# Optimization experiments

Hardware: AMD Instinct MI355X
Metric: run time of the kernel (lower is better)

The kernel has to match this reference:

```python
import jax, jax.numpy as jnp
import numpy as np

N, E, B = 50000, 800000, 128
IN, HID, OUT = 15, 256, 128
EPS = 1e-5


def setup_inputs() -> dict:
    key = jax.random.key(0)
    ks = jax.random.split(key, 16)
    x = jax.random.normal(ks[0], (N, IN), jnp.float32)
    edge_index = jax.random.randint(ks[1], (2, E), 0, N, jnp.int32)
    batch = jnp.sort(jax.random.randint(ks[2], (N,), 0, B, jnp.int32))
    w = lambda k, i, o: jax.random.normal(k, (i, o), jnp.float32) * (1.0 / np.sqrt(i))
    return {
        "x": x, "edge_index": edge_index, "batch": batch,
        "Wl1": w(ks[3], IN, HID), "Wr1": w(ks[4], IN, HID), "b1": jnp.zeros((HID,), jnp.float32),
        "g1": jnp.ones((HID,), jnp.float32), "bt1": jnp.zeros((HID,), jnp.float32),
        "Wl2": w(ks[5], HID, HID), "Wr2": w(ks[6], HID, HID), "b2": jnp.zeros((HID,), jnp.float32),
        "g2": jnp.ones((HID,), jnp.float32), "bt2": jnp.zeros((HID,), jnp.float32),
        "Wl3": w(ks[7], HID, HID), "Wr3": w(ks[8], HID, HID), "b3": jnp.zeros((HID,), jnp.float32),
        "g3": jnp.ones((HID,), jnp.float32), "bt3": jnp.zeros((HID,), jnp.float32),
        "Wl4": w(ks[9], HID, OUT), "Wr4": w(ks[10], HID, OUT), "b4": jnp.zeros((OUT,), jnp.float32),
        "g4": jnp.ones((OUT,), jnp.float32), "bt4": jnp.zeros((OUT,), jnp.float32),
    }


def _sage(x, src, dst, Wl, Wr, b):
    # mean-aggregate source-node features at each target, then two GEMMs
    msg = x[src]                                            # (E, d)
    agg = jax.ops.segment_sum(msg, dst, num_segments=N)     # (N, d)
    cnt = jax.ops.segment_sum(jnp.ones((src.shape[0],), x.dtype), dst, num_segments=N)
    mean = agg / jnp.clip(cnt, 1.0)[:, None]
    return mean @ Wl + x @ Wr + b


def _ln(x, g, b):
    mu = jnp.mean(x, axis=-1, keepdims=True)
    var = jnp.mean(jnp.square(x - mu), axis=-1, keepdims=True)
    return (x - mu) * jax.lax.rsqrt(var + EPS) * g + b


def reference(x, edge_index, batch,
              Wl1, Wr1, b1, g1, bt1,
              Wl2, Wr2, b2, g2, bt2,
              Wl3, Wr3, b3, g3, bt3,
              Wl4, Wr4, b4, g4, bt4):
    src, dst = edge_index[0], edge_index[1]
    gelu = lambda h: jax.nn.gelu(h, approximate=False)
    h = gelu(_ln(_sage(x, src, dst, Wl1, Wr1, b1), g1, bt1))
    h = gelu(_ln(_sage(h, src, dst, Wl2, Wr2, b2), g2, bt2))
    h = gelu(_ln(_sage(h, src, dst, Wl3, Wr3, b3), g3, bt3))
    h = gelu(_ln(_sage(h, src, dst, Wl4, Wr4, b4), g4, bt4))
    # global mean pool per patch
    s = jax.ops.segment_sum(h, batch, num_segments=B)        # (B, out)
    c = jax.ops.segment_sum(jnp.ones((N,), h.dtype), batch, num_segments=B)
    return s / jnp.clip(c, 1.0)[:, None]
```

## Files before the change

kernel.cpp:

```cpp
#include <hip/hip_runtime.h>
#include <math.h>

constexpr int Nn   = 50000;
constexpr int Ee   = 800000;
constexpr int Bb   = 128;
constexpr int INF  = 15;
constexpr int HID  = 256;
constexpr int OUTF = 128;

constexpr int NCB   = (Nn + 255) / 256;
constexpr int CHUNK = 4096;
constexpr int NB1   = (Ee + CHUNK - 1) / CHUNK;
constexpr int SCANN = NCB * NB1;

typedef __attribute__((ext_vector_type(8))) __bf16 bf16x8;
typedef __attribute__((ext_vector_type(4))) float  f32x4;

__device__ __forceinline__ float gelu_f(float v) {
    return 0.5f * v * (1.0f + erff(v * 0.7071067811865475f));
}

__device__ __forceinline__ unsigned short f2bf(float f) {
    union { float f; unsigned int u; } v; v.f = f;
    unsigned int r = v.u + 0x7fffu + ((v.u >> 16) & 1u);
    return (unsigned short)(r >> 16);
}

__device__ __forceinline__ float bflo(unsigned int p) { return __uint_as_float(p << 16); }
__device__ __forceinline__ float bfhi(unsigned int p) { return __uint_as_float(p & 0xffff0000u); }


__global__ void k_sortA(const int* __restrict__ dst, int* __restrict__ Gcnt) {
    __shared__ int cnt[NCB];
    int tid = threadIdx.x, blk = blockIdx.x;
    for (int i = tid; i < NCB; i += 256) cnt[i] = 0;
    __syncthreads();
    int base = blk * CHUNK;
    for (int i = 0; i < CHUNK; i += 256) {
        int e = base + i + tid;
        if (e < Ee) atomicAdd(&cnt[dst[e] >> 8], 1);
    }
    __syncthreads();
    for (int i = tid; i < NCB; i += 256) Gcnt[i * NB1 + blk] = cnt[i];
}

__global__ void k_gscan_partial(const int* __restrict__ in, int* __restrict__ partial, int n) {
    __shared__ int s[256];
    int tid = threadIdx.x, i = blockIdx.x * 256 + tid;
    s[tid] = (i < n) ? in[i] : 0;
    __syncthreads();
    for (int off = 128; off; off >>= 1) {
        if (tid < off) s[tid] += s[tid + off];
        __syncthreads();
    }
    if (tid == 0) partial[blockIdx.x] = s[0];
}

__global__ void k_gscan_mid(int* __restrict__ partial, int nb) {
    __shared__ int s[256];
    int tid = threadIdx.x;
    int v = (tid < nb) ? partial[tid] : 0;
    s[tid] = v;
    __syncthreads();
    for (int off = 1; off < 256; off <<= 1) {
        int t = (tid >= off) ? s[tid - off] : 0;
        __syncthreads();
        s[tid] += t;
        __syncthreads();
    }
    if (tid < nb) partial[tid] = s[tid] - v;
}

__global__ void k_gscan_final(const int* __restrict__ in, const int* __restrict__ partial,
                              int* __restrict__ out, int n) {
    __shared__ int s[256];
    int tid = threadIdx.x, i = blockIdx.x * 256 + tid;
    int v = (i < n) ? in[i] : 0;
    s[tid] = v;
    __syncthreads();
    for (int off = 1; off < 256; off <<= 1) {
        int t = (tid >= off) ? s[tid - off] : 0;
        __syncthreads();
        s[tid] += t;
        __syncthreads();
    }
    if (i < n) out[i] = s[tid] - v + partial[blockIdx.x];
}

__global__ void k_sortC(const int* __restrict__ dst, const int* __restrict__ srcv,
                        const int* __restrict__ Goff, unsigned int* __restrict__ pairs) {
    __shared__ int cur[NCB];
    int tid = threadIdx.x, blk = blockIdx.x;
    for (int i = tid; i < NCB; i += 256) cur[i] = Goff[i * NB1 + blk];
    __syncthreads();
    int base = blk * CHUNK;
    for (int i = 0; i < CHUNK; i += 256) {
        int e = base + i + tid;
        if (e < Ee) {
            int d = dst[e];
            int p = atomicAdd(&cur[d >> 8], 1);
            pairs[p] = ((unsigned int)(d & 255) << 16) | (unsigned int)srcv[e];
        }
    }
}

__global__ void k_sortD(const unsigned int* __restrict__ pairs, const int* __restrict__ Goff,
                        int* __restrict__ offs, int* __restrict__ srcs, float* __restrict__ invc) {
    __shared__ int fcnt[256];
    __shared__ int fbase[256];
    __shared__ int s[256];
    int tid = threadIdx.x, cb = blockIdx.x;
    int cbase = Goff[cb * NB1];
    int cend = (cb + 1 < NCB) ? Goff[(cb + 1) * NB1] : Ee;
    fcnt[tid] = 0;
    __syncthreads();
    for (int e = cbase + tid; e < cend; e += 256)
        atomicAdd(&fcnt[pairs[e] >> 16], 1);
    __syncthreads();
    int v = fcnt[tid];
    s[tid] = v;
    __syncthreads();
    for (int off = 1; off < 256; off <<= 1) {
        int t = (tid >= off) ? s[tid - off] : 0;
        __syncthreads();
        s[tid] += t;
        __syncthreads();
    }
    fbase[tid] = cbase + s[tid] - v;
    int node = cb * 256 + tid;
    if (node < Nn) {
        offs[node] = fbase[tid];
        invc[node] = 1.0f / (float)(v > 1 ? v : 1);
    }
    __syncthreads();
    fcnt[tid] = fbase[tid];
    __syncthreads();
    for (int e = cbase + tid; e < cend; e += 256) {
        unsigned int pv = pairs[e];
        int p = atomicAdd(&fcnt[pv >> 16], 1);
        srcs[p] = (int)(pv & 0xFFFFu);
    }
}

__global__ void k_bsearch(const int* __restrict__ batch, int* __restrict__ boff,
                          int* __restrict__ offs) {
    int b = threadIdx.x;
    if (b <= Bb) {
        int lo = 0, hi = Nn;
        while (lo < hi) {
            int mid = (lo + hi) >> 1;
            if (batch[mid] < b) lo = mid + 1; else hi = mid;
        }
        boff[b] = lo;
    }
    if (b == 0) offs[Nn] = Ee;
}


template <int NOUT>
__global__ void k_prepW(const float* __restrict__ Wl, const float* __restrict__ Wr,
                        uint4* __restrict__ outw) {
    constexpr int NT = NOUT / 16;
    int G = blockIdx.x * 256 + threadIdx.x;
    int per = 2 * NT * 64;
    int S = G / per, rem = G % per;
    int lane = rem & 63, sT = rem >> 6;
    int s = sT / NT, T = sT % NT;
    int q = lane >> 4, m = lane & 15;
    int k0 = S * 64 + s * 32 + q * 8;
    int nc = T * 16 + m;
    union { uint4 u; unsigned short h[8]; } pk;
#pragma unroll
    for (int j = 0; j < 8; j++) {
        int kk = k0 + j;
        float wv = (kk < 256) ? Wl[kk * NOUT + nc] : Wr[(kk - 256) * NOUT + nc];
        pk.h[j] = f2bf(wv);
    }
    outw[G] = pk.u;
}

__global__ void k_prepW1(const float* __restrict__ Wl, const float* __restrict__ Wr,
                         uint4* __restrict__ outw) {
    int G = blockIdx.x * 256 + threadIdx.x;
    int T = G >> 6, lane = G & 63;
    int q = lane >> 4, m = lane & 15;
    int nc = T * 16 + m;
    union { uint4 u; unsigned short h[8]; } pk;
#pragma unroll
    for (int j = 0; j < 8; j++) {
        int k = q * 8 + j;
        float wv;
        if (k < 15)       wv = Wl[k * HID + nc];
        else if (k == 15) wv = 0.0f;
        else if (k < 31)  wv = Wr[(k - 16) * HID + nc];
        else              wv = 0.0f;
        pk.h[j] = f2bf(wv);
    }
    outw[G] = pk.u;
}


__global__ void k_prep1(const float* __restrict__ x, const int* __restrict__ offs,
                        const int* __restrict__ srcs, const float* __restrict__ invc,
                        unsigned short* __restrict__ A1) {
    int node = blockIdx.x * 16 + (threadIdx.x >> 4);
    int f = threadIdx.x & 15;
    int s0 = offs[node], s1 = offs[node + 1];
    float acc = 0.0f;
    for (int i = s0; i < s1; i++) {
        int s = srcs[i];
        if (f < 15) acc += x[s * INF + f];
    }
    unsigned short mv = (f < 15) ? f2bf(acc * invc[node]) : (unsigned short)0;
    unsigned short xv = (f < 15) ? f2bf(x[(size_t)node * INF + f]) : (unsigned short)0;
    A1[(size_t)node * 32 + f] = mv;
    A1[(size_t)node * 32 + 16 + f] = xv;
}


__global__ void k_agg256_bf(const uint4* __restrict__ h4, const int* __restrict__ offs,
                            const int* __restrict__ srcs, const float* __restrict__ invc,
                            uint4* __restrict__ mean4) {
    int node = blockIdx.x * 4 + (threadIdx.x >> 6);
    int lane = threadIdx.x & 63;
    int sub = lane >> 5, q = lane & 31;
    int s0 = offs[node], s1 = offs[node + 1];
    int deg = s1 - s0;
    int dcap = deg < 64 ? deg : 64;
    int myidx = (lane < deg) ? srcs[s0 + lane] : 0;
    float a[8] = {};
    int i = 0;
    for (; i + 4 <= dcap; i += 4) {
        int sA = __shfl(myidx, i + sub);
        int sB = __shfl(myidx, i + 2 + sub);
        uint4 vA = h4[(size_t)sA * 32 + q];
        uint4 vB = h4[(size_t)sB * 32 + q];
        a[0] += bflo(vA.x); a[1] += bfhi(vA.x);
        a[2] += bflo(vA.y); a[3] += bfhi(vA.y);
        a[4] += bflo(vA.z); a[5] += bfhi(vA.z);
        a[6] += bflo(vA.w); a[7] += bfhi(vA.w);
        a[0] += bflo(vB.x); a[1] += bfhi(vB.x);
        a[2] += bflo(vB.y); a[3] += bfhi(vB.y);
        a[4] += bflo(vB.z); a[5] += bfhi(vB.z);
        a[6] += bflo(vB.w); a[7] += bfhi(vB.w);
    }
    if (i + 2 <= dcap) {
        int sA = __shfl(myidx, i + sub);
        uint4 vA = h4[(size_t)sA * 32 + q];
        a[0] += bflo(vA.x); a[1] += bfhi(vA.x);
        a[2] += bflo(vA.y); a[3] += bfhi(vA.y);
        a[4] += bflo(vA.z); a[5] += bfhi(vA.z);
        a[6] += bflo(vA.w); a[7] += bfhi(vA.w);
        i += 2;
    }
    if (i < dcap && sub == 0) {
        int sA = __shfl(myidx, i);
        uint4 vA = h4[(size_t)sA * 32 + q];
        a[0] += bflo(vA.x); a[1] += bfhi(vA.x);
        a[2] += bflo(vA.y); a[3] += bfhi(vA.y);
        a[4] += bflo(vA.z); a[5] += bfhi(vA.z);
        a[6] += bflo(vA.w); a[7] += bfhi(vA.w);
    }
    for (int j = 64; j + 1 < deg; j += 2) {
        int s = srcs[s0 + j + sub];
        uint4 v = h4[(size_t)s * 32 + q];
        a[0] += bflo(v.x); a[1] += bfhi(v.x);
        a[2] += bflo(v.y); a[3] += bfhi(v.y);
        a[4] += bflo(v.z); a[5] += bfhi(v.z);
        a[6] += bflo(v.w); a[7] += bfhi(v.w);
    }
    if (deg > 64 && ((deg - 64) & 1) && sub == 0) {
        int s = srcs[s1 - 1];
        uint4 v = h4[(size_t)s * 32 + q];
        a[0] += bflo(v.x); a[1] += bfhi(v.x);
        a[2] += bflo(v.y); a[3] += bfhi(v.y);
        a[4] += bflo(v.z); a[5] += bfhi(v.z);
        a[6] += bflo(v.w); a[7] += bfhi(v.w);
    }
#pragma unroll
    for (int j = 0; j < 8; j++) a[j] += __shfl_xor(a[j], 32);
    if (sub == 0) {
        float ic = invc[node];
        uint4 o;
        o.x = (unsigned int)f2bf(a[0] * ic) | ((unsigned int)f2bf(a[1] * ic) << 16);
        o.y = (unsigned int)f2bf(a[2] * ic) | ((unsigned int)f2bf(a[3] * ic) << 16);
        o.z = (unsigned int)f2bf(a[4] * ic) | ((unsigned int)f2bf(a[5] * ic) << 16);
        o.w = (unsigned int)f2bf(a[6] * ic) | ((unsigned int)f2bf(a[7] * ic) << 16);
        mean4[(size_t)node * 32 + q] = o;
    }
}


template <int NOUT, bool F32OUT>
__global__ __launch_bounds__(256) void k_gemm_mfma(
    const unsigned short* __restrict__ Am,
    const unsigned short* __restrict__ Ah,
    const uint4* __restrict__ Wfrag,
    const float* __restrict__ bias, const float* __restrict__ g,
    const float* __restrict__ bt, void* __restrict__ outp, int n) {
    constexpr int NT = NOUT / 16;
    constexpr int CT = NT / 4;
    __shared__ float lnbuf[2][4][64];
    int tid = threadIdx.x;
    int w = tid >> 6, lane = tid & 63;
    int q = lane >> 4, m = lane & 15;
    int rowbase = blockIdx.x * 64;

    f32x4 acc[4][CT];
#pragma unroll
    for (int i = 0; i < 4; i++)
#pragma unroll
        for (int t = 0; t < CT; t++) acc[i][t] = (f32x4)0.f;

    union U { uint4 u; bf16x8 b; };
    U a[2][4], b[2][CT];

    auto loadA = [&](int p, U* ar) {
        const unsigned short* A = (p < 8) ? Am : Ah;
        int kk = ((p >> 1) & 3) * 64 + (p & 1) * 32 + q * 8;
#pragma unroll
        for (int i = 0; i < 4; i++)
            ar[i].u = *(const uint4*)(A + (size_t)(rowbase + i * 16 + m) * 256 + kk);
    };
    auto loadB = [&](int p, U* br) {
#pragma unroll
        for (int t = 0; t < CT; t++)
            br[t].u = Wfrag[(size_t)(p * NT + w * CT + t) * 64 + lane];
    };

    loadA(0, a[0]);
    loadB(0, b[0]);
#pragma unroll
    for (int p = 0; p < 16; p++) {
        int cur = p & 1, nxt = cur ^ 1;
        if (p < 15) {
            loadA(p + 1, a[nxt]);
            loadB(p + 1, b[nxt]);
        }
#pragma unroll
        for (int i = 0; i < 4; i++)
#pragma unroll
            for (int t = 0; t < CT; t++)
                acc[i][t] = __builtin_amdgcn_mfma_f32_16x16x32_bf16(
                    a[cur][i].b, b[cur][t].b, acc[i][t], 0, 0, 0);
    }

    int col0 = w * CT * 16;
    float bv[CT], gv[CT], btv[CT];
#pragma unroll
    for (int t = 0; t < CT; t++) {
        int c = col0 + t * 16 + m;
        bv[t] = bias[c]; gv[t] = g[c]; btv[t] = bt[c];
    }
#pragma unroll
    for (int i = 0; i < 4; i++) {
#pragma unroll
        for (int r = 0; r < 4; r++) {
            float s1 = 0.f, s2 = 0.f;
#pragma unroll
            for (int t = 0; t < CT; t++) {
                float v = acc[i][t][r] + bv[t];
                acc[i][t][r] = v;
                s1 += v; s2 += v * v;
            }
#pragma unroll
            for (int o = 1; o < 16; o <<= 1) {
                s1 += __shfl_xor(s1, o);
                s2 += __shfl_xor(s2, o);
            }
            if (m == 0) {
                int row = i * 16 + q * 4 + r;
                lnbuf[0][w][row] = s1;
                lnbuf[1][w][row] = s2;
            }
        }
    }
    __syncthreads();
#pragma unroll
    for (int i = 0; i < 4; i++) {
#pragma unroll
        for (int r = 0; r < 4; r++) {
            int rit = i * 16 + q * 4 + r;
            float ts1 = lnbuf[0][0][rit] + lnbuf[0][1][rit] + lnbuf[0][2][rit] + lnbuf[0][3][rit];
            float ts2 = lnbuf[1][0][rit] + lnbuf[1][1][rit] + lnbuf[1][2][rit] + lnbuf[1][3][rit];
            float mu  = ts1 * (1.0f / NOUT);
            float var = ts2 * (1.0f / NOUT) - mu * mu;
            float rs  = 1.0f / sqrtf(var + 1e-5f);
            int row = rowbase + rit;
            if (row < n) {
#pragma unroll
                for (int t = 0; t < CT; t++) {
                    int c = col0 + t * 16 + m;
                    float y = (acc[i][t][r] - mu) * rs * gv[t] + btv[t];
                    float res = gelu_f(y);
                    if (F32OUT) ((float*)outp)[(size_t)row * NOUT + c] = res;
                    else ((unsigned short*)outp)[(size_t)row * NOUT + c] = f2bf(res);
                }
            }
        }
    }
}


__global__ __launch_bounds__(256) void k_gemm_mfma1(
    const unsigned short* __restrict__ A1, const uint4* __restrict__ Wfrag,
    const float* __restrict__ bias, const float* __restrict__ g,
    const float* __restrict__ bt, unsigned short* __restrict__ outp, int n) {
    constexpr int NT = 16, CT = 4;
    __shared__ float lnbuf[2][4][64];
    int tid = threadIdx.x;
    int w = tid >> 6, lane = tid & 63;
    int q = lane >> 4, m = lane & 15;
    int rowbase = blockIdx.x * 64;

    union U { uint4 u; bf16x8 b; };
    U a[4], b[CT];
#pragma unroll
    for (int i = 0; i < 4; i++) {
        int row = rowbase + i * 16 + m;
        a[i].u = (row < n) ? *(const uint4*)(A1 + (size_t)row * 32 + q * 8)
                           : make_uint4(0u, 0u, 0u, 0u);
    }
#pragma unroll
    for (int t = 0; t < CT; t++)
        b[t].u = Wfrag[(size_t)(w * CT + t) * 64 + lane];

    f32x4 acc[4][CT];
#pragma unroll
    for (int i = 0; i < 4; i++)
#pragma unroll
        for (int t = 0; t < CT; t++)
            acc[i][t] = __builtin_amdgcn_mfma_f32_16x16x32_bf16(
                a[i].b, b[t].b, (f32x4)0.f, 0, 0, 0);

    int col0 = w * CT * 16;
    float bv[CT], gv[CT], btv[CT];
#pragma unroll
    for (int t = 0; t < CT; t++) {
        int c = col0 + t * 16 + m;
        bv[t] = bias[c]; gv[t] = g[c]; btv[t] = bt[c];
    }
#pragma unroll
    for (int i = 0; i < 4; i++) {
#pragma unroll
        for (int r = 0; r < 4; r++) {
            float s1 = 0.f, s2 = 0.f;
#pragma unroll
            for (int t = 0; t < CT; t++) {
                float v = acc[i][t][r] + bv[t];
                acc[i][t][r] = v;
                s1 += v; s2 += v * v;
            }
#pragma unroll
            for (int o = 1; o < 16; o <<= 1) {
                s1 += __shfl_xor(s1, o);
                s2 += __shfl_xor(s2, o);
            }
            if (m == 0) {
                int row = i * 16 + q * 4 + r;
                lnbuf[0][w][row] = s1;
                lnbuf[1][w][row] = s2;
            }
        }
    }
    __syncthreads();
#pragma unroll
    for (int i = 0; i < 4; i++) {
#pragma unroll
        for (int r = 0; r < 4; r++) {
            int rit = i * 16 + q * 4 + r;
            float ts1 = lnbuf[0][0][rit] + lnbuf[0][1][rit] + lnbuf[0][2][rit] + lnbuf[0][3][rit];
            float ts2 = lnbuf[1][0][rit] + lnbuf[1][1][rit] + lnbuf[1][2][rit] + lnbuf[1][3][rit];
            float mu  = ts1 * (1.0f / HID);
            float var = ts2 * (1.0f / HID) - mu * mu;
            float rs  = 1.0f / sqrtf(var + 1e-5f);
            int row = rowbase + rit;
            if (row < n) {
#pragma unroll
                for (int t = 0; t < CT; t++) {
                    int c = col0 + t * 16 + m;
                    float y = (acc[i][t][r] - mu) * rs * gv[t] + btv[t];
                    outp[(size_t)row * HID + c] = f2bf(gelu_f(y));
                }
            }
        }
    }
}


__global__ __launch_bounds__(1024) void k_pool(const float* __restrict__ h,
                                               const int* __restrict__ boff,
                                               float* __restrict__ out) {
    __shared__ float red[8][128];
    int b = blockIdx.x, tid = threadIdx.x;
    int j = tid & 127, grp = tid >> 7;
    int s0 = boff[b], s1 = boff[b + 1];
    float a0 = 0.f, a1 = 0.f, a2 = 0.f, a3 = 0.f;
    int i = s0 + grp;
    for (; i + 24 < s1; i += 32) {
        a0 += h[(size_t)i * OUTF + j];
        a1 += h[(size_t)(i + 8) * OUTF + j];
        a2 += h[(size_t)(i + 16) * OUTF + j];
        a3 += h[(size_t)(i + 24) * OUTF + j];
    }
    for (; i < s1; i += 8) a0 += h[(size_t)i * OUTF + j];
    red[grp][j] = (a0 + a1) + (a2 + a3);
    __syncthreads();
    if (tid < 128) {
        float s = ((red[0][tid] + red[1][tid]) + (red[2][tid] + red[3][tid]))
                + ((red[4][tid] + red[5][tid]) + (red[6][tid] + red[7][tid]));
        int c = s1 - s0;
        out[b * OUTF + tid] = s / fmaxf((float)c, 1.0f);
    }
}


extern "C" void kernel_launch(void* const* d_in, const int* in_sizes, int n_in,
                              void* d_out, int out_size, void* d_ws, size_t ws_size,
                              hipStream_t stream) {
    const float* x     = (const float*)d_in[0];
    const int*   ei    = (const int*)d_in[1];
    const int*   src   = ei;
    const int*   dst   = ei + Ee;
    const int*   batch = (const int*)d_in[2];
    const float* Wl1 = (const float*)d_in[3];
    const float* Wr1 = (const float*)d_in[4];
    const float* b1  = (const float*)d_in[5];
    const float* g1  = (const float*)d_in[6];
    const float* bt1 = (const float*)d_in[7];
    const float* Wl2 = (const float*)d_in[8];
    const float* Wr2 = (const float*)d_in[9];
    const float* b2  = (const float*)d_in[10];
    const float* g2  = (const float*)d_in[11];
    const float* bt2 = (const float*)d_in[12];
    const float* Wl3 = (const float*)d_in[13];
    const float* Wr3 = (const float*)d_in[14];
    const float* b3  = (const float*)d_in[15];
    const float* g3  = (const float*)d_in[16];
    const float* bt3 = (const float*)d_in[17];
    const float* Wl4 = (const float*)d_in[18];
    const float* Wr4 = (const float*)d_in[19];
    const float* b4  = (const float*)d_in[20];
    const float* g4  = (const float*)d_in[21];
    const float* bt4 = (const float*)d_in[22];
    float* out = (float*)d_out;

    char* ws = (char*)d_ws;
    size_t off = 0;
    auto alloc = [&](size_t bytes) -> char* {
        char* p = ws + off;
        off = (off + bytes + 255) & ~(size_t)255;
        return p;
    };
    int*   offs    = (int*)alloc((size_t)(Nn + 1) * 4);
    int*   srcs    = (int*)alloc((size_t)Ee * 4);
    float* invc    = (float*)alloc((size_t)Nn * 4);
    int*   boff    = (int*)alloc((size_t)(Bb + 1) * 4);
    unsigned int* pairs = (unsigned int*)alloc((size_t)Ee * 4);
    int*   Gcnt    = (int*)alloc((size_t)SCANN * 4);
    int*   Goff    = (int*)alloc((size_t)SCANN * 4);
    int*   partial = (int*)alloc(256 * 4);
    unsigned short* A1    = (unsigned short*)alloc((size_t)Nn * 32 * 2);
    unsigned short* meanb = (unsigned short*)alloc((size_t)Nn * HID * 2);
    unsigned short* hA    = (unsigned short*)alloc((size_t)Nn * HID * 2);
    unsigned short* hB    = (unsigned short*)alloc((size_t)Nn * HID * 2);
    float* hOut    = (float*)alloc((size_t)Nn * OUTF * 4);
    uint4* W1f     = (uint4*)alloc((size_t)32 * HID * 2);
    uint4* W2f     = (uint4*)alloc((size_t)512 * HID * 2);
    uint4* W3f     = (uint4*)alloc((size_t)512 * HID * 2);
    uint4* W4f     = (uint4*)alloc((size_t)512 * OUTF * 2);

    int nbScan = (SCANN + 255) / 256;
    k_sortA<<<NB1, 256, 0, stream>>>(dst, Gcnt);
    k_gscan_partial<<<nbScan, 256, 0, stream>>>(Gcnt, partial, SCANN);
    k_gscan_mid<<<1, 256, 0, stream>>>(partial, nbScan);
    k_gscan_final<<<nbScan, 256, 0, stream>>>(Gcnt, partial, Goff, SCANN);
    k_sortC<<<NB1, 256, 0, stream>>>(dst, src, Goff, pairs);
    k_sortD<<<NCB, 256, 0, stream>>>(pairs, Goff, offs, srcs, invc);
    k_bsearch<<<1, 256, 0, stream>>>(batch, boff, offs);

    k_prepW1<<<4, 256, 0, stream>>>(Wl1, Wr1, W1f);
    k_prepW<256><<<64, 256, 0, stream>>>(Wl2, Wr2, W2f);
    k_prepW<256><<<64, 256, 0, stream>>>(Wl3, Wr3, W3f);
    k_prepW<128><<<32, 256, 0, stream>>>(Wl4, Wr4, W4f);

    int gb = (Nn + 63) / 64;
    k_prep1<<<Nn / 16, 256, 0, stream>>>(x, offs, srcs, invc, A1);
    k_gemm_mfma1<<<gb, 256, 0, stream>>>(A1, W1f, b1, g1, bt1, hA, Nn);
    k_agg256_bf<<<Nn / 4, 256, 0, stream>>>((const uint4*)hA, offs, srcs, invc, (uint4*)meanb);
    k_gemm_mfma<256, false><<<gb, 256, 0, stream>>>(meanb, hA, W2f, b2, g2, bt2, hB, Nn);
    k_agg256_bf<<<Nn / 4, 256, 0, stream>>>((const uint4*)hB, offs, srcs, invc, (uint4*)meanb);
    k_gemm_mfma<256, false><<<gb, 256, 0, stream>>>(meanb, hB, W3f, b3, g3, bt3, hA, Nn);
    k_agg256_bf<<<Nn / 4, 256, 0, stream>>>((const uint4*)hA, offs, srcs, invc, (uint4*)meanb);
    k_gemm_mfma<128, true><<<gb, 256, 0, stream>>>(meanb, hA, W4f, b4, g4, bt4, hOut, Nn);
    k_pool<<<Bb, 1024, 0, stream>>>(hOut, boff, out);
}
```

Measured before the change: 566.6 us.

## Stage GEMM A tiles through LDS and unroll aggregation gather by eight

The MFMA GEMM kernel now loads the 64x256 bf16 A tile once per phase with coalesced global loads into padded shared memory (stride 33 uint4 to avoid bank conflicts). All four waves then read their fragments from LDS, where previously each wave fetched the same A rows from global memory. The neighbour-aggregation kernel's first loop is unrolled to issue four gathers per iteration, giving more memory-level parallelism. The trade-offs are extra barriers, about 33KB of LDS per block (which may lower occupancy), and the loss of the register double-buffering of A loads.

```diff
diff --git a/kernel.cpp b/kernel.cpp
--- a/kernel.cpp
+++ b/kernel.cpp
@@ -218,6 +218,13 @@
 }
 
 
+__device__ __forceinline__ void acc8(float* a, uint4 v) {
+    a[0] += bflo(v.x); a[1] += bfhi(v.x);
+    a[2] += bflo(v.y); a[3] += bfhi(v.y);
+    a[4] += bflo(v.z); a[5] += bfhi(v.z);
+    a[6] += bflo(v.w); a[7] += bfhi(v.w);
+}
+
 __global__ void k_agg256_bf(const uint4* __restrict__ h4, const int* __restrict__ offs,
                             const int* __restrict__ srcs, const float* __restrict__ invc,
                             uint4* __restrict__ mean4) {
@@ -230,52 +237,45 @@
     int myidx = (lane < deg) ? srcs[s0 + lane] : 0;
     float a[8] = {};
     int i = 0;
-    for (; i + 4 <= dcap; i += 4) {
+    for (; i + 8 <= dcap; i += 8) {
+        int sA = __shfl(myidx, i + sub);
+        int sB = __shfl(myidx, i + 2 + sub);
+        int sC = __shfl(myidx, i + 4 + sub);
+        int sD = __shfl(myidx, i + 6 + sub);
+        uint4 vA = h4[(size_t)sA * 32 + q];
+        uint4 vB = h4[(size_t)sB * 32 + q];
+        uint4 vC = h4[(size_t)sC * 32 + q];
+        uint4 vD = h4[(size_t)sD * 32 + q];
+        acc8(a, vA); acc8(a, vB); acc8(a, vC); acc8(a, vD);
+    }
+    if (i + 4 <= dcap) {
         int sA = __shfl(myidx, i + sub);
         int sB = __shfl(myidx, i + 2 + sub);
         uint4 vA = h4[(size_t)sA * 32 + q];
         uint4 vB = h4[(size_t)sB * 32 + q];
-        a[0] += bflo(vA.x); a[1] += bfhi(vA.x);
-        a[2] += bflo(vA.y); a[3] += bfhi(vA.y);
-        a[4] += bflo(vA.z); a[5] += bfhi(vA.z);
-        a[6] += bflo(vA.w); a[7] += bfhi(vA.w);
-        a[0] += bflo(vB.x); a[1] += bfhi(vB.x);
-        a[2] += bflo(vB.y); a[3] += bfhi(vB.y);
-        a[4] += bflo(vB.z); a[5] += bfhi(vB.z);
-        a[6] += bflo(vB.w); a[7] += bfhi(vB.w);
+        acc8(a, vA); acc8(a, vB);
+        i += 4;
     }
     if (i + 2 <= dcap) {
         int sA = __shfl(myidx, i + sub);
         uint4 vA = h4[(size_t)sA * 32 + q];
-        a[0] += bflo(vA.x); a[1] += bfhi(vA.x);
-        a[2] += bflo(vA.y); a[3] += bfhi(vA.y);
-        a[4] += bflo(vA.z); a[5] += bfhi(vA.z);
-        a[6] += bflo(vA.w); a[7] += bfhi(vA.w);
+        acc8(a, vA);
         i += 2;
     }
     if (i < dcap && sub == 0) {
         int sA = __shfl(myidx, i);
         uint4 vA = h4[(size_t)sA * 32 + q];
-        a[0] += bflo(vA.x); a[1] += bfhi(vA.x);
-        a[2] += bflo(vA.y); a[3] += bfhi(vA.y);
-        a[4] += bflo(vA.z); a[5] += bfhi(vA.z);
-        a[6] += bflo(vA.w); a[7] += bfhi(vA.w);
+        acc8(a, vA);
     }
     for (int j = 64; j + 1 < deg; j += 2) {
         int s = srcs[s0 + j + sub];
         uint4 v = h4[(size_t)s * 32 + q];
-        a[0] += bflo(v.x); a[1] += bfhi(v.x);
-        a[2] += bflo(v.y); a[3] += bfhi(v.y);
-        a[4] += bflo(v.z); a[5] += bfhi(v.z);
-        a[6] += bflo(v.w); a[7] += bfhi(v.w);
+        acc8(a, v);
     }
     if (deg > 64 && ((deg - 64) & 1) && sub == 0) {
         int s = srcs[s1 - 1];
         uint4 v = h4[(size_t)s * 32 + q];
-        a[0] += bflo(v.x); a[1] += bfhi(v.x);
-        a[2] += bflo(v.y); a[3] += bfhi(v.y);
-        a[4] += bflo(v.z); a[5] += bfhi(v.z);
-        a[6] += bflo(v.w); a[7] += bfhi(v.w);
+        acc8(a, v);
     }
 #pragma unroll
     for (int j = 0; j < 8; j++) a[j] += __shfl_xor(a[j], 32);
@@ -300,6 +300,8 @@
     const float* __restrict__ bt, void* __restrict__ outp, int n) {
     constexpr int NT = NOUT / 16;
     constexpr int CT = NT / 4;
+    constexpr int SROW = 33;
+    __shared__ __align__(16) uint4 Abuf[64 * SROW];
     __shared__ float lnbuf[2][4][64];
     int tid = threadIdx.x;
     int w = tid >> 6, lane = tid & 63;
@@ -313,14 +315,23 @@
         for (int t = 0; t < CT; t++) acc[i][t] = (f32x4)0.f;
 
     union U { uint4 u; bf16x8 b; };
-    U a[2][4], b[2][CT];
-
-    auto loadA = [&](int p, U* ar) {
-        const unsigned short* A = (p < 8) ? Am : Ah;
-        int kk = ((p >> 1) & 3) * 64 + (p & 1) * 32 + q * 8;
-#pragma unroll
-        for (int i = 0; i < 4; i++)
-            ar[i].u = *(const uint4*)(A + (size_t)(rowbase + i * 16 + m) * 256 + kk);
+    U a[4], breg[2][CT];
+
+    auto stage = [&](const unsigned short* A) {
+        const uint4* Ag = (const uint4*)A + (size_t)rowbase * 32;
+        uint4 v[8];
+#pragma unroll
+        for (int j = 0; j < 8; j++) {
+            int c = j * 256 + tid;
+            int row = c >> 5;
+            v[j] = (rowbase + row < n) ? Ag[c] : make_uint4(0u, 0u, 0u, 0u);
+        }
+#pragma unroll
+        for (int j = 0; j < 8; j++) {
+            int c = j * 256 + tid;
+            int row = c >> 5, kc = c & 31;
+            Abuf[row * SROW + kc] = v[j];
+        }
     };
     auto loadB = [&](int p, U* br) {
 #pragma unroll
@@ -328,21 +339,32 @@
             br[t].u = Wfrag[(size_t)(p * NT + w * CT + t) * 64 + lane];
     };
 
-    loadA(0, a[0]);
-    loadB(0, b[0]);
-#pragma unroll
-    for (int p = 0; p < 16; p++) {
-        int cur = p & 1, nxt = cur ^ 1;
-        if (p < 15) {
-            loadA(p + 1, a[nxt]);
-            loadB(p + 1, b[nxt]);
-        }
-#pragma unroll
-        for (int i = 0; i < 4; i++)
-#pragma unroll
-            for (int t = 0; t < CT; t++)
-                acc[i][t] = __builtin_amdgcn_mfma_f32_16x16x32_bf16(
-                    a[cur][i].b, b[cur][t].b, acc[i][t], 0, 0, 0);
+    stage(Am);
+    loadB(0, breg[0]);
+    __syncthreads();
+
+#pragma unroll
+    for (int ph = 0; ph < 2; ph++) {
+        if (ph == 1) {
+            __syncthreads();
+            stage(Ah);
+            __syncthreads();
+        }
+#pragma unroll
+        for (int pp = 0; pp < 8; pp++) {
+            int p = ph * 8 + pp;
+            int cur = p & 1, nxt = cur ^ 1;
+#pragma unroll
+            for (int i = 0; i < 4; i++)
+                a[i].u = Abuf[(i * 16 + m) * SROW + pp * 4 + q];
+            if (p < 15) loadB(p + 1, breg[nxt]);
+#pragma unroll
+            for (int i = 0; i < 4; i++)
+#pragma unroll
+                for (int t = 0; t < CT; t++)
+                    acc[i][t] = __builtin_amdgcn_mfma_f32_16x16x32_bf16(
+                        a[i].b, breg[cur][t].b, acc[i][t], 0, 0, 0);
+        }
     }
 
     int col0 = w * CT * 16;
```

Result: faster. 513.5 us (-9.4%).
